# Kernel tuning notes

Hardware: AMD Instinct MI355X
Metric: run time of the kernel (lower is better)

Reference implementation:

```python
import jax, jax.numpy as jnp
import numpy as np
from jax import lax

B, D, H, W = 8, 256, 56, 56
DH = 32            # d_head
HEADS = D // DH    # 8
WIN = 7            # window size
TOPK = 8           # top-k windows
DM = 4 * D         # mlp hidden = 1024
EPS = 1e-5


def bn(x, g, b, m, v):
    # inference-mode BatchNorm2d over channel dim of NCHW
    return g[:, None, None] * (x - m[:, None, None]) * lax.rsqrt(v[:, None, None] + EPS) + b[:, None, None]


def conv1x1(x, w):
    return jnp.einsum('bchw,oc->bohw', x, w)


def setup_inputs() -> dict:
    key = jax.random.key(0)
    ks = jax.random.split(key, 24)
    s = 0.05
    return {
        'x': jax.random.normal(ks[0], (B, D, H, W), jnp.float32),
        'g1': jax.random.uniform(ks[1], (D,)) + 0.5,
        'b1': jax.random.normal(ks[2], (D,)) * s,
        'm1': jax.random.normal(ks[3], (D,)) * s,
        'v1': jax.random.uniform(ks[4], (D,)) + 0.5,
        'W_qkv': jax.random.normal(ks[5], (3 * D, D)) * s,
        'W_merge': jax.random.normal(ks[6], (D, D)) * s,
        'b_merge': jax.random.normal(ks[7], (D,)) * s,
        'W1': jax.random.normal(ks[8], (DM, D)) * s,
        'g2': jax.random.uniform(ks[9], (DM,)) + 0.5,
        'b2': jax.random.normal(ks[10], (DM,)) * s,
        'm2': jax.random.normal(ks[11], (DM,)) * s,
        'v2': jax.random.uniform(ks[12], (DM,)) + 0.5,
        'Wdw': jax.random.normal(ks[13], (DM, 1, 3, 3)) * s,
        'g3': jax.random.uniform(ks[14], (DM,)) + 0.5,
        'b3': jax.random.normal(ks[15], (DM,)) * s,
        'm3': jax.random.normal(ks[16], (DM,)) * s,
        'v3': jax.random.uniform(ks[17], (DM,)) + 0.5,
        'W2': jax.random.normal(ks[18], (D, DM)) * s,
        'g4': jax.random.uniform(ks[19], (D,)) + 0.5,
        'b4': jax.random.normal(ks[20], (D,)) * s,
        'm4': jax.random.normal(ks[21], (D,)) * s,
        'v4': jax.random.uniform(ks[22], (D,)) + 0.5,
    }


def _forward(x, g1, b1, m1, v1, W_qkv, W_merge, b_merge,
             W1, g2, b2, m2, v2, Wdw, g3, b3, m3, v3, W2, g4, b4, m4, v4):
    b_, d, Hh, Ww = x.shape
    nh, nw = Hh // WIN, Ww // WIN
    nWnd, ww = nh * nw, WIN * WIN

    # qkv projection: BN -> GELU -> 1x1 conv
    h = jax.nn.gelu(bn(x, g1, b1, m1, v1), approximate=False)
    qkv = conv1x1(h, W_qkv)
    q, k, v = jnp.split(qkv, 3, axis=1)  # each [b, d, H, W]

    def part(t):  # -> [b, heads, nWnd, ww, dh]
        t = t.reshape(b_, HEADS, DH, nh, WIN, nw, WIN)
        return jnp.transpose(t, (0, 1, 3, 5, 4, 6, 2)).reshape(b_, HEADS, nWnd, ww, DH)

    qw, kw, vw = part(q), part(k), part(v)

    # window-level routing: mean-pooled q/k per window, top-k window selection
    def pool(t):  # [b, d, H, W] -> [b, nWnd, d]
        t = t.reshape(b_, d, nh, WIN, nw, WIN).mean(axis=(3, 5))
        return t.reshape(b_, d, nWnd).transpose(0, 2, 1)

    qr, kr = pool(q), pool(k)
    aff = jnp.einsum('bnd,bmd->bnm', qr, kr)        # [b, nWnd, nWnd]
    idx = lax.top_k(aff, TOPK)[1]                    # [b, nWnd, TOPK]

    def gath(t, i):  # t [heads, nWnd, ww, dh], i [nWnd, TOPK]
        return t[:, i]  # [heads, nWnd, TOPK, ww, dh]

    kg = jax.vmap(gath)(kw, idx).reshape(b_, HEADS, nWnd, TOPK * ww, DH)
    vg = jax.vmap(gath)(vw, idx).reshape(b_, HEADS, nWnd, TOPK * ww, DH)

    scores = jnp.einsum('bhnqd,bhnkd->bhnqk', qw, kg) / jnp.sqrt(jnp.float32(DH))
    attn = jax.nn.softmax(scores, axis=-1)
    out = jnp.einsum('bhnqk,bhnkd->bhnqd', attn, vg)  # [b, heads, nWnd, ww, dh]

    # un-partition back to [b, d, H, W]
    out = out.reshape(b_, HEADS, nh, nw, WIN, WIN, DH)
    msg = jnp.transpose(out, (0, 1, 6, 2, 4, 3, 5)).reshape(b_, d, Hh, Ww)

    # merge (1x1 conv with bias) + residual
    x = x + conv1x1(msg, W_merge) + b_merge[None, :, None, None]

    # MB mlp block: 1x1 -> BN -> GELU -> dw3x3 -> BN -> GELU -> 1x1 -> BN
    h2 = conv1x1(x, W1)
    h2 = jax.nn.gelu(bn(h2, g2, b2, m2, v2), approximate=False)
    h2 = lax.conv_general_dilated(h2, Wdw, (1, 1), 'SAME',
                                  feature_group_count=DM,
                                  dimension_numbers=('NCHW', 'OIHW', 'NCHW'))
    h2 = jax.nn.gelu(bn(h2, g3, b3, m3, v3), approximate=False)
    h2 = conv1x1(h2, W2)
    h2 = bn(h2, g4, b4, m4, v4)
    return x + h2


def reference(x, g1, b1, m1, v1, W_qkv, W_merge, b_merge,
              W1, g2, b2, m2, v2, Wdw, g3, b3, m3, v3, W2, g4, b4, m4, v4):
    return _forward(x, g1, b1, m1, v1, W_qkv, W_merge, b_merge,
                    W1, g2, b2, m2, v2, Wdw, g3, b3, m3, v3, W2, g4, b4, m4, v4)
```

## Files before the change

kernel.cpp:

```cpp
#include <hip/hip_runtime.h>
#include <cstdint>
#include <cstddef>

#define BB 8
#define PP 3136
#define EPSV 1e-5f

using bf16x8 = __attribute__((ext_vector_type(8))) short;
using f32x4  = __attribute__((ext_vector_type(4))) float;

__device__ __forceinline__ float bf2f(unsigned short u) {
    union { float f; unsigned int i; } c; c.i = ((unsigned int)u) << 16; return c.f;
}
__device__ __forceinline__ unsigned short f2bf(float f) {
    union { float f; unsigned int i; } c; c.f = f;
    unsigned int r = c.i + 0x7FFFu + ((c.i >> 16) & 1u);
    return (unsigned short)(r >> 16);
}
__device__ __forceinline__ float gelu_f(float t) {
    return 0.5f * t * (1.0f + erff(t * 0.70710678118654752440f));
}
__device__ __forceinline__ void async16(const void* g, void* s) {
    __builtin_amdgcn_global_load_lds(
        (const __attribute__((address_space(1))) unsigned int*)g,
        (__attribute__((address_space(3))) unsigned int*)s, 16, 0, 0);
}

__global__ __launch_bounds__(256) void cvt_bf16_k(const float* __restrict__ src,
    unsigned short* __restrict__ dst, int n)
{
    int i = blockIdx.x * 256 + threadIdx.x;
    if (i < n) dst[i] = f2bf(src[i]);
}

__global__ __launch_bounds__(256) void transin_k(const float* __restrict__ x,
    const float* __restrict__ g1, const float* __restrict__ b1,
    const float* __restrict__ m1, const float* __restrict__ v1,
    float* __restrict__ x_pm, unsigned short* __restrict__ h_bf)
{
    __shared__ float tile[64][65];
    __shared__ float gam[64], bet[64], mu[64], rst[64];
    const int p0 = blockIdx.x * 64, c0 = blockIdx.y * 64, b = blockIdx.z;
    const int t = threadIdx.x;
    if (t < 64) { int c = c0 + t; gam[t] = g1[c]; bet[t] = b1[c]; mu[t] = m1[c]; rst[t] = rsqrtf(v1[c] + EPSV); }
    {
        int cl = t >> 2, px = (t & 3) * 16;
        const float* src = x + ((size_t)(b * 256 + c0 + cl)) * PP + p0 + px;
        #pragma unroll
        for (int i4 = 0; i4 < 4; i4++) {
            float4 r0 = *(const float4*)(src + i4 * 4);
            tile[cl][px + i4*4 + 0] = r0.x; tile[cl][px + i4*4 + 1] = r0.y;
            tile[cl][px + i4*4 + 2] = r0.z; tile[cl][px + i4*4 + 3] = r0.w;
        }
    }
    __syncthreads();
    {
        int pl = t >> 2, cb = (t & 3) * 16;
        float raw[16], hg[16];
        #pragma unroll
        for (int i = 0; i < 16; i++) {
            float vv = tile[cb + i][pl];
            raw[i] = vv;
            hg[i] = gelu_f(gam[cb + i] * (vv - mu[cb + i]) * rst[cb + i] + bet[cb + i]);
        }
        size_t off = ((size_t)b * PP + p0 + pl) * 256 + c0 + cb;
        float* xd = x_pm + off;
        #pragma unroll
        for (int i4 = 0; i4 < 4; i4++) {
            float4 o; o.x = raw[i4*4]; o.y = raw[i4*4+1]; o.z = raw[i4*4+2]; o.w = raw[i4*4+3];
            *(float4*)(xd + i4 * 4) = o;
        }
        unsigned int uw[8];
        #pragma unroll
        for (int j = 0; j < 8; j++)
            uw[j] = (unsigned int)f2bf(hg[2*j]) | ((unsigned int)f2bf(hg[2*j+1]) << 16);
        uint4* hd = (uint4*)(h_bf + off);
        uint4 h0; h0.x = uw[0]; h0.y = uw[1]; h0.z = uw[2]; h0.w = uw[3];
        uint4 h1; h1.x = uw[4]; h1.y = uw[5]; h1.z = uw[6]; h1.w = uw[7];
        hd[0] = h0; hd[1] = h1;
    }
}

template<int EPI>
__global__ __launch_bounds__(256) void gemm_mfma_k(
    const unsigned short* __restrict__ Aact,
    const unsigned short* __restrict__ Wbf,
    const int K, const int Mout,
    void* __restrict__ C1, void* __restrict__ C2,
    const float* __restrict__ e0, const float* __restrict__ e1,
    const float* __restrict__ e2, const float* __restrict__ e3,
    const float* __restrict__ resid)
{
    __shared__ __align__(16) unsigned short As[4][128 * 32];
    __shared__ __align__(16) unsigned short Bs[4][128 * 32];
    const int tid = threadIdx.x;
    const int w = tid >> 6, lane = tid & 63, g = lane >> 4, l15 = lane & 15;
    const int wm = w >> 1, wn = w & 1;
    const size_t row0 = (size_t)blockIdx.x * 128;
    const int n0 = blockIdx.y * 128;

    const int srow = tid >> 2;
    const int scb  = tid & 3;

    const f32x4 vzero = {0.f, 0.f, 0.f, 0.f};
    f32x4 acc[4][4];
    #pragma unroll
    for (int mf = 0; mf < 4; mf++)
        #pragma unroll
        for (int nf = 0; nf < 4; nf++) acc[mf][nf] = vzero;

    const int NT = K >> 5;

    auto STAGE = [&](int s) {
        const int k0 = s << 5;
        unsigned short* Ad = &As[s & 3][0];
        unsigned short* Bd = &Bs[s & 3][0];
        #pragma unroll
        for (int r = 0; r < 2; r++) {
            int row = r * 64 + srow;
            int cbp = scb ^ ((row >> 1) & 3);
            async16(Aact + (row0 + row) * K + k0 + cbp * 8, Ad + r * 2048 + w * 512);
            async16(Wbf + (size_t)(n0 + row) * K + k0 + cbp * 8, Bd + r * 2048 + w * 512);
        }
    };
    auto COMPUTE = [&](int t) {
        const unsigned short* Ab = As[t & 3];
        const unsigned short* Bb = Bs[t & 3];
        bf16x8 af[4], bfr[4];
        #pragma unroll
        for (int mf = 0; mf < 4; mf++) {
            int row = wm * 64 + mf * 16 + l15;
            int gb = g ^ ((row >> 1) & 3);
            af[mf] = *(const bf16x8*)&Ab[row * 32 + gb * 8];
        }
        #pragma unroll
        for (int nf = 0; nf < 4; nf++) {
            int row = wn * 64 + nf * 16 + l15;
            int gb = g ^ ((row >> 1) & 3);
            bfr[nf] = *(const bf16x8*)&Bb[row * 32 + gb * 8];
        }
        #pragma unroll
        for (int mf = 0; mf < 4; mf++)
            #pragma unroll
            for (int nf = 0; nf < 4; nf++)
                acc[mf][nf] = __builtin_amdgcn_mfma_f32_16x16x32_bf16(af[mf], bfr[nf], acc[mf][nf], 0, 0, 0);
    };

    STAGE(0); STAGE(1); STAGE(2);
    for (int t = 0; t < NT - 2; ++t) {
        asm volatile("s_waitcnt vmcnt(8)" ::: "memory");
        __builtin_amdgcn_s_barrier();
        if (t + 3 < NT) STAGE(t + 3);
        COMPUTE(t);
    }
    asm volatile("s_waitcnt vmcnt(4)" ::: "memory");
    __builtin_amdgcn_s_barrier();
    COMPUTE(NT - 2);
    asm volatile("s_waitcnt vmcnt(0)" ::: "memory");
    __builtin_amdgcn_s_barrier();
    COMPUTE(NT - 1);

    #pragma unroll
    for (int nf = 0; nf < 4; nf++) {
        const int mcol = n0 + wn * 64 + nf * 16 + l15;
        float gam = 0.f, bet = 0.f, mu = 0.f, rs = 0.f, bias = 0.f;
        if (EPI == 2 || EPI == 3) {
            gam = e0[mcol]; bet = e1[mcol]; mu = e2[mcol]; rs = rsqrtf(e3[mcol] + EPSV);
        }
        if (EPI == 1) bias = e0[mcol];
        #pragma unroll
        for (int mf = 0; mf < 4; mf++) {
            #pragma unroll
            for (int r = 0; r < 4; r++) {
                const size_t prow = row0 + wm * 64 + mf * 16 + g * 4 + r;
                const size_t off = prow * Mout + mcol;
                float a = acc[mf][nf][r];
                if (EPI == 0) {
                    if (mcol < 256) a *= 0.17677669529663687f;
                    ((unsigned short*)C1)[off] = f2bf(a);
                } else if (EPI == 1) {
                    float y = a + bias + resid[off];
                    ((float*)C1)[off] = y;
                    ((unsigned short*)C2)[off] = f2bf(y);
                } else if (EPI == 2) {
                    float y = gam * (a - mu) * rs + bet;
                    ((unsigned short*)C1)[off] = f2bf(gelu_f(y));
                } else {
                    float y = gam * (a - mu) * rs + bet + resid[off];
                    ((float*)C1)[off] = y;
                }
            }
        }
    }
}

__global__ __launch_bounds__(256) void poolh_k(const float* __restrict__ x_pm,
    const float* __restrict__ g1, const float* __restrict__ b1,
    const float* __restrict__ m1, const float* __restrict__ v1,
    float* __restrict__ ph)
{
    __shared__ float part[4][256];
    __shared__ float gam[256], bet[256], mu[256], rst[256];
    const int n = blockIdx.x, b = blockIdx.y, t = threadIdx.x;
    gam[t] = g1[t]; bet[t] = b1[t]; mu[t] = m1[t]; rst[t] = rsqrtf(v1[t] + EPSV);
    __syncthreads();
    const int c4 = (t & 63) * 4, pg = t >> 6;
    float s0 = 0.f, s1 = 0.f, s2 = 0.f, s3 = 0.f;
    for (int j = pg; j < 49; j += 4) {
        int p = ((n >> 3) * 7 + j / 7) * 56 + (n & 7) * 7 + j % 7;
        float4 vx = *(const float4*)(x_pm + ((size_t)b * PP + p) * 256 + c4);
        s0 += gelu_f(gam[c4+0] * (vx.x - mu[c4+0]) * rst[c4+0] + bet[c4+0]);
        s1 += gelu_f(gam[c4+1] * (vx.y - mu[c4+1]) * rst[c4+1] + bet[c4+1]);
        s2 += gelu_f(gam[c4+2] * (vx.z - mu[c4+2]) * rst[c4+2] + bet[c4+2]);
        s3 += gelu_f(gam[c4+3] * (vx.w - mu[c4+3]) * rst[c4+3] + bet[c4+3]);
    }
    part[pg][c4 + 0] = s0; part[pg][c4 + 1] = s1; part[pg][c4 + 2] = s2; part[pg][c4 + 3] = s3;
    __syncthreads();
    float tot = part[0][t] + part[1][t] + part[2][t] + part[3][t];
    ph[((size_t)b * 64 + n) * 256 + t] = tot * (1.0f / 49.0f);
}

__global__ __launch_bounds__(256) void qrkr_k(const float* __restrict__ ph,
    const float* __restrict__ Wqkv, float* __restrict__ qr, float* __restrict__ kr)
{
    __shared__ float row[256];
    const int n = blockIdx.x, b = blockIdx.y, t = threadIdx.x;
    row[t] = ph[((size_t)b * 64 + n) * 256 + t];
    __syncthreads();
    const float* wq = Wqkv + (size_t)t * 256;
    const float* wk = Wqkv + (size_t)(256 + t) * 256;
    float aq = 0.f, ak = 0.f;
    #pragma unroll 4
    for (int k = 0; k < 256; k += 4) {
        float4 a4 = *(const float4*)(wq + k);
        float4 b4 = *(const float4*)(wk + k);
        aq += row[k]*a4.x + row[k+1]*a4.y + row[k+2]*a4.z + row[k+3]*a4.w;
        ak += row[k]*b4.x + row[k+1]*b4.y + row[k+2]*b4.z + row[k+3]*b4.w;
    }
    qr[((size_t)b * 64 + n) * 256 + t] = aq;
    kr[((size_t)b * 64 + n) * 256 + t] = ak;
}

__global__ __launch_bounds__(64) void topk_k(const float* __restrict__ qr,
    const float* __restrict__ kr, int* __restrict__ idxb)
{
    const int n = blockIdx.x, b_ = blockIdx.y;
    const int tid = threadIdx.x;
    __shared__ float qrow[256];
    *reinterpret_cast<float4*>(&qrow[tid * 4]) =
        *reinterpret_cast<const float4*>(qr + ((size_t)(b_ * 64) + n) * 256 + tid * 4);
    __syncthreads();
    const float* kp = kr + ((size_t)(b_ * 64) + tid) * 256;
    float av = 0.f;
    #pragma unroll 4
    for (int c = 0; c < 256; c++) av = fmaf(qrow[c], kp[c], av);
    for (int t = 0; t < 8; t++) {
        float v = av; int id = tid;
        #pragma unroll
        for (int off = 32; off; off >>= 1) {
            float v2 = __shfl_xor(v, off);
            int id2 = __shfl_xor(id, off);
            if (v2 > v || (v2 == v && id2 < id)) { v = v2; id = id2; }
        }
        if (tid == 0) idxb[((b_ * 64) + n) * 8 + t] = id;
        if (tid == id) av = -1e30f;
    }
}

__global__ __launch_bounds__(256) void attn_mfma_k(const unsigned short* __restrict__ qkv,
    const int* __restrict__ idxb, unsigned short* __restrict__ msg)
{
    __shared__ __align__(16) unsigned short Ks[64 * 40];
    __shared__ __align__(16) unsigned short Vt[32 * 72];
    __shared__ __align__(16) unsigned short Pr[4][16 * 72];
    const int n = blockIdx.x, h = blockIdx.y, b = blockIdx.z;
    const int tid = threadIdx.x;
    const int w = tid >> 6, lane = tid & 63, g = lane >> 4, l15 = lane & 15;

    for (int e = tid; e < 64 * 40; e += 256) Ks[e] = 0;
    for (int e = tid; e < 32 * 72; e += 256) Vt[e] = 0;

    const int iq = w * 16 + l15;
    bf16x8 qf = {0, 0, 0, 0, 0, 0, 0, 0};
    if (iq < 49) {
        int p = ((n >> 3) * 7 + iq / 7) * 56 + (n & 7) * 7 + iq % 7;
        qf = *(const bf16x8*)(qkv + ((size_t)b * PP + p) * 768 + h * 32 + g * 8);
    }
    const f32x4 vzero = {0.f, 0.f, 0.f, 0.f};
    f32x4 o0 = vzero, o1 = vzero;
    float mrow = -1e30f, lrow = 0.f;

    for (int t = 0; t < 8; t++) {
        const int wsrc = idxb[((b * 64) + n) * 8 + t];
        const int sy0 = (wsrc >> 3) * 7, sx0 = (wsrc & 7) * 7;
        __syncthreads();
        if (tid < 196) {
            int j = tid >> 2, c8 = (tid & 3) * 8;
            int p = (sy0 + j / 7) * 56 + sx0 + j % 7;
            const unsigned short* srcp = qkv + ((size_t)b * PP + p) * 768 + 256 + h * 32 + c8;
            uint4 kk = *(const uint4*)srcp;
            *(uint4*)&Ks[j * 40 + c8] = kk;
            uint4 vv = *(const uint4*)(srcp + 256);
            const unsigned short* pv = (const unsigned short*)&vv;
            #pragma unroll
            for (int jj = 0; jj < 8; jj++) {
                int dh = c8 + jj;
                Vt[dh * 72 + (j ^ (((dh >> 3) & 3) << 3))] = pv[jj];
            }
        }
        __syncthreads();
        f32x4 s[4];
        #pragma unroll
        for (int nf = 0; nf < 4; nf++) {
            bf16x8 kf = *(const bf16x8*)&Ks[(nf * 16 + l15) * 40 + g * 8];
            s[nf] = __builtin_amdgcn_mfma_f32_16x16x32_bf16(kf, qf, vzero, 0, 0, 0);
        }
        float sv[16];
        #pragma unroll
        for (int nf = 0; nf < 4; nf++)
            #pragma unroll
            for (int r = 0; r < 4; r++) {
                int j = nf * 16 + g * 4 + r;
                sv[nf * 4 + r] = (j < 49) ? s[nf][r] : -1e30f;
            }
        float wmx = sv[0];
        #pragma unroll
        for (int e = 1; e < 16; e++) wmx = fmaxf(wmx, sv[e]);
        wmx = fmaxf(wmx, __shfl_xor(wmx, 16));
        wmx = fmaxf(wmx, __shfl_xor(wmx, 32));
        float mn = fmaxf(mrow, wmx);
        float corr = __expf(mrow - mn);
        mrow = mn;
        float rsum = 0.f;
        #pragma unroll
        for (int e = 0; e < 16; e++) { float pe = __expf(sv[e] - mn); sv[e] = pe; rsum += pe; }
        rsum += __shfl_xor(rsum, 16);
        rsum += __shfl_xor(rsum, 32);
        lrow = lrow * corr + rsum;
        #pragma unroll
        for (int r = 0; r < 4; r++) { o0[r] *= corr; o1[r] *= corr; }
        #pragma unroll
        for (int nf = 0; nf < 4; nf++) {
            uint2 pw;
            pw.x = (unsigned)f2bf(sv[nf*4+0]) | ((unsigned)f2bf(sv[nf*4+1]) << 16);
            pw.y = (unsigned)f2bf(sv[nf*4+2]) | ((unsigned)f2bf(sv[nf*4+3]) << 16);
            *(uint2*)&Pr[w][l15 * 72 + nf * 16 + g * 4] = pw;
        }
        asm volatile("s_waitcnt lgkmcnt(0)" ::: "memory");
        #pragma unroll
        for (int ks = 0; ks < 2; ks++) {
            const int j0 = ks * 32 + g * 8;
            bf16x8 pf  = *(const bf16x8*)&Pr[w][l15 * 72 + j0];
            bf16x8 vf0 = *(const bf16x8*)&Vt[l15 * 72 + (j0 ^ (((l15 >> 3) & 1) << 3))];
            bf16x8 vf1 = *(const bf16x8*)&Vt[(16 + l15) * 72 + (j0 ^ ((2 + (l15 >> 3)) << 3))];
            o0 = __builtin_amdgcn_mfma_f32_16x16x32_bf16(vf0, pf, o0, 0, 0, 0);
            o1 = __builtin_amdgcn_mfma_f32_16x16x32_bf16(vf1, pf, o1, 0, 0, 0);
        }
    }
    if (iq < 49) {
        float inv = 1.0f / lrow;
        int p = ((n >> 3) * 7 + iq / 7) * 56 + (n & 7) * 7 + iq % 7;
        size_t off = ((size_t)b * PP + p) * 256 + h * 32;
        uint2 w0, w1;
        w0.x = (unsigned)f2bf(o0[0]*inv) | ((unsigned)f2bf(o0[1]*inv) << 16);
        w0.y = (unsigned)f2bf(o0[2]*inv) | ((unsigned)f2bf(o0[3]*inv) << 16);
        w1.x = (unsigned)f2bf(o1[0]*inv) | ((unsigned)f2bf(o1[1]*inv) << 16);
        w1.y = (unsigned)f2bf(o1[2]*inv) | ((unsigned)f2bf(o1[3]*inv) << 16);
        *(uint2*)(msg + off + g * 4) = w0;
        *(uint2*)(msg + off + 16 + g * 4) = w1;
    }
}

__global__ __launch_bounds__(256) void dwconv_k(const unsigned short* __restrict__ in,
    const float* __restrict__ w9,
    const float* __restrict__ g3, const float* __restrict__ b3,
    const float* __restrict__ m3, const float* __restrict__ v3,
    unsigned short* __restrict__ out)
{
    __shared__ __align__(16) unsigned short tl[100 * 64];
    const int sx = blockIdx.x % 7, sy = blockIdx.x / 7;
    const int c0 = blockIdx.y * 64, b = blockIdx.z;
    const int t = threadIdx.x;
    for (int e = t; e < 800; e += 256) {
        int pos = e >> 3, c8 = (e & 7) * 8;
        int iy = sy * 8 + pos / 10 - 1, ix = sx * 8 + pos % 10 - 1;
        uint4 val = {0u, 0u, 0u, 0u};
        if (iy >= 0 && iy < 56 && ix >= 0 && ix < 56)
            val = *(const uint4*)(in + ((size_t)b * PP + iy * 56 + ix) * 1024 + c0 + c8);
        *(uint4*)&tl[pos * 64 + c8] = val;
    }
    __syncthreads();
    const int c2 = (t & 31) * 2, pg = t >> 5;
    const int c = c0 + c2;
    float w0[9], w1[9];
    #pragma unroll
    for (int i = 0; i < 9; i++) { w0[i] = w9[c * 9 + i]; w1[i] = w9[(c + 1) * 9 + i]; }
    const float ga0 = g3[c], be0 = b3[c], mu0 = m3[c], rs0 = rsqrtf(v3[c] + EPSV);
    const float ga1 = g3[c+1], be1 = b3[c+1], mu1 = m3[c+1], rs1 = rsqrtf(v3[c+1] + EPSV);
    #pragma unroll
    for (int q = 0; q < 8; q++) {
        int pos = pg * 8 + q, y = pos >> 3, xq = pos & 7;
        float s0 = 0.f, s1 = 0.f;
        #pragma unroll
        for (int dy = 0; dy < 3; dy++)
            #pragma unroll
            for (int dx = 0; dx < 3; dx++) {
                unsigned int u = *(const unsigned int*)&tl[((y + dy) * 10 + xq + dx) * 64 + c2];
                s0 = fmaf(bf2f((unsigned short)(u & 0xffffu)), w0[dy * 3 + dx], s0);
                s1 = fmaf(bf2f((unsigned short)(u >> 16)), w1[dy * 3 + dx], s1);
            }
        float y0 = gelu_f(ga0 * (s0 - mu0) * rs0 + be0);
        float y1 = gelu_f(ga1 * (s1 - mu1) * rs1 + be1);
        unsigned int ow = (unsigned int)f2bf(y0) | ((unsigned int)f2bf(y1) << 16);
        size_t off = ((size_t)b * PP + (sy * 8 + y) * 56 + sx * 8 + xq) * 1024 + c;
        *(unsigned int*)&out[off] = ow;
    }
}

__global__ __launch_bounds__(256) void transout_k(const float* __restrict__ out_pm,
    float* __restrict__ dout)
{
    __shared__ float tile[64][65];
    const int p0 = blockIdx.x * 64, c0 = blockIdx.y * 64, b = blockIdx.z;
    const int t = threadIdx.x;
    {
        int pl = t >> 2, cx = (t & 3) * 16;
        const float* src = out_pm + ((size_t)b * PP + p0 + pl) * 256 + c0 + cx;
        #pragma unroll
        for (int i4 = 0; i4 < 4; i4++) {
            float4 vv = *(const float4*)(src + i4 * 4);
            tile[pl][cx + i4*4 + 0] = vv.x; tile[pl][cx + i4*4 + 1] = vv.y;
            tile[pl][cx + i4*4 + 2] = vv.z; tile[pl][cx + i4*4 + 3] = vv.w;
        }
    }
    __syncthreads();
    {
        int cl = t >> 2, px = (t & 3) * 16;
        float* dst = dout + ((size_t)(b * 256 + c0 + cl)) * PP + p0 + px;
        #pragma unroll
        for (int i4 = 0; i4 < 4; i4++) {
            float4 o;
            o.x = tile[px + i4*4 + 0][cl]; o.y = tile[px + i4*4 + 1][cl];
            o.z = tile[px + i4*4 + 2][cl]; o.w = tile[px + i4*4 + 3][cl];
            *(float4*)(dst + i4 * 4) = o;
        }
    }
}

extern "C" void kernel_launch(void* const* d_in, const int* in_sizes, int n_in,
                              void* d_out, int out_size, void* d_ws, size_t ws_size,
                              hipStream_t stream)
{
    const float* x      = (const float*)d_in[0];
    const float* g1     = (const float*)d_in[1];
    const float* b1     = (const float*)d_in[2];
    const float* m1     = (const float*)d_in[3];
    const float* v1     = (const float*)d_in[4];
    const float* Wqkv   = (const float*)d_in[5];
    const float* Wmerge = (const float*)d_in[6];
    const float* bmerge = (const float*)d_in[7];
    const float* W1     = (const float*)d_in[8];
    const float* g2     = (const float*)d_in[9];
    const float* b2     = (const float*)d_in[10];
    const float* m2     = (const float*)d_in[11];
    const float* v2     = (const float*)d_in[12];
    const float* Wdw    = (const float*)d_in[13];
    const float* g3     = (const float*)d_in[14];
    const float* b3     = (const float*)d_in[15];
    const float* m3     = (const float*)d_in[16];
    const float* v3     = (const float*)d_in[17];
    const float* W2     = (const float*)d_in[18];
    const float* g4     = (const float*)d_in[19];
    const float* b4     = (const float*)d_in[20];
    const float* m4     = (const float*)d_in[21];
    const float* v4     = (const float*)d_in[22];

    char* ws = (char*)d_ws;
    float*          x_pm   = (float*)(ws + 0);
    float*          x2_pm  = (float*)(ws + 25690112);
    unsigned short* x2_bf  = (unsigned short*)(ws + 51380224);
    unsigned short* qkv_pm = (unsigned short*)(ws + 64225280);
    unsigned short* msg_pm = (unsigned short*)(ws + 102760448);
    unsigned short* t1     = (unsigned short*)(ws + 115605504);
    unsigned short* h_bf   = t1;
    unsigned short* t2     = (unsigned short*)(ws + 166985728);
    float*          ph     = (float*)(ws + 218365952);
    float*          qr     = (float*)(ws + 218890240);
    float*          kr     = (float*)(ws + 219414528);
    int*            idxb   = (int*)(ws + 219938816);
    unsigned short* Wqkv_b = (unsigned short*)(ws + 219955200);
    unsigned short* Wmrg_b = (unsigned short*)(ws + 220348416);
    unsigned short* W1_b   = (unsigned short*)(ws + 220479488);
    unsigned short* W2_b   = (unsigned short*)(ws + 221003776);
    float*          out_pm = x_pm;
    if (ws_size < 221528064) return;

    cvt_bf16_k<<<768, 256, 0, stream>>>(Wqkv, Wqkv_b, 196608);
    cvt_bf16_k<<<256, 256, 0, stream>>>(Wmerge, Wmrg_b, 65536);
    cvt_bf16_k<<<1024, 256, 0, stream>>>(W1, W1_b, 262144);
    cvt_bf16_k<<<1024, 256, 0, stream>>>(W2, W2_b, 262144);
    transin_k<<<dim3(49, 4, BB), 256, 0, stream>>>(x, g1, b1, m1, v1, x_pm, h_bf);
    gemm_mfma_k<0><<<dim3(196, 6), 256, 0, stream>>>(h_bf, Wqkv_b, 256, 768,
        qkv_pm, nullptr, nullptr, nullptr, nullptr, nullptr, nullptr);
    poolh_k<<<dim3(64, BB), 256, 0, stream>>>(x_pm, g1, b1, m1, v1, ph);
    qrkr_k<<<dim3(64, BB), 256, 0, stream>>>(ph, Wqkv, qr, kr);
    topk_k<<<dim3(64, BB), 64, 0, stream>>>(qr, kr, idxb);
    attn_mfma_k<<<dim3(64, 8, BB), 256, 0, stream>>>(qkv_pm, idxb, msg_pm);
    gemm_mfma_k<1><<<dim3(196, 2), 256, 0, stream>>>(msg_pm, Wmrg_b, 256, 256,
        x2_pm, x2_bf, bmerge, nullptr, nullptr, nullptr, x_pm);
    gemm_mfma_k<2><<<dim3(196, 8), 256, 0, stream>>>(x2_bf, W1_b, 256, 1024,
        t1, nullptr, g2, b2, m2, v2, nullptr);
    dwconv_k<<<dim3(49, 16, BB), 256, 0, stream>>>(t1, Wdw, g3, b3, m3, v3, t2);
    gemm_mfma_k<3><<<dim3(196, 2), 256, 0, stream>>>(t2, W2_b, 1024, 256,
        out_pm, nullptr, g4, b4, m4, v4, x2_pm);
    transout_k<<<dim3(49, 4, BB), 256, 0, stream>>>(out_pm, (float*)d_out);
}
```

Measured before the change: 345.5 us.

## Stage GEMM epilogue through LDS, use tanh GELU, fuse weight casts, prefetch attention K/V

Several changes at once. The GEMM epilogue now goes through shared memory so each thread writes contiguous 16-byte vectors instead of scattered 2/4-byte stores. The GEMM pipeline shrinks from 4-stage to 2-stage buffering with __syncthreads, which cuts LDS to about 34 KB but reduces the prefetch depth. Exact erf GELU is replaced by a tanh/sigmoid approximation in transin, the W1 epilogue and dwconv, which changes numerics. The four weight-conversion launches are merged into one, and the attention kernel prefetches the next window's K/V into registers while the current one is processed.

After: 340.9 us. About the same (-1.3%).

```diff
diff --git a/kernel.cpp b/kernel.cpp
--- a/kernel.cpp
+++ b/kernel.cpp
@@ -5,6 +5,7 @@
 #define BB 8
 #define PP 3136
 #define EPSV 1e-5f
+#define SCQK 0.17677669529663687f
 
 using bf16x8 = __attribute__((ext_vector_type(8))) short;
 using f32x4  = __attribute__((ext_vector_type(4))) float;
@@ -20,17 +21,35 @@
 __device__ __forceinline__ float gelu_f(float t) {
     return 0.5f * t * (1.0f + erff(t * 0.70710678118654752440f));
 }
+__device__ __forceinline__ float gelu_fast(float x) {
+    float z = 1.5957691216057308f * (x + 0.044715f * x * x * x);
+    return x / (1.0f + __expf(-z));
+}
 __device__ __forceinline__ void async16(const void* g, void* s) {
     __builtin_amdgcn_global_load_lds(
         (const __attribute__((address_space(1))) unsigned int*)g,
         (__attribute__((address_space(3))) unsigned int*)s, 16, 0, 0);
 }
-
-__global__ __launch_bounds__(256) void cvt_bf16_k(const float* __restrict__ src,
-    unsigned short* __restrict__ dst, int n)
+__device__ __forceinline__ uint4 pack8(const float* v) {
+    uint4 o;
+    o.x = (unsigned)f2bf(v[0]) | ((unsigned)f2bf(v[1]) << 16);
+    o.y = (unsigned)f2bf(v[2]) | ((unsigned)f2bf(v[3]) << 16);
+    o.z = (unsigned)f2bf(v[4]) | ((unsigned)f2bf(v[5]) << 16);
+    o.w = (unsigned)f2bf(v[6]) | ((unsigned)f2bf(v[7]) << 16);
+    return o;
+}
+
+__global__ __launch_bounds__(256) void cvt_all_k(
+    const float* __restrict__ Wq, const float* __restrict__ Wm,
+    const float* __restrict__ W1, const float* __restrict__ W2,
+    unsigned short* __restrict__ dq, unsigned short* __restrict__ dm,
+    unsigned short* __restrict__ d1, unsigned short* __restrict__ d2)
 {
     int i = blockIdx.x * 256 + threadIdx.x;
-    if (i < n) dst[i] = f2bf(src[i]);
+    if (i < 196608) dq[i] = f2bf(Wq[i]);
+    else if (i < 262144) dm[i - 196608] = f2bf(Wm[i - 196608]);
+    else if (i < 524288) d1[i - 262144] = f2bf(W1[i - 262144]);
+    else d2[i - 524288] = f2bf(W2[i - 524288]);
 }
 
 __global__ __launch_bounds__(256) void transin_k(const float* __restrict__ x,
@@ -61,7 +80,7 @@
         for (int i = 0; i < 16; i++) {
             float vv = tile[cb + i][pl];
             raw[i] = vv;
-            hg[i] = gelu_f(gam[cb + i] * (vv - mu[cb + i]) * rst[cb + i] + bet[cb + i]);
+            hg[i] = gelu_fast(gam[cb + i] * (vv - mu[cb + i]) * rst[cb + i] + bet[cb + i]);
         }
         size_t off = ((size_t)b * PP + p0 + pl) * 256 + c0 + cb;
         float* xd = x_pm + off;
@@ -70,14 +89,9 @@
             float4 o; o.x = raw[i4*4]; o.y = raw[i4*4+1]; o.z = raw[i4*4+2]; o.w = raw[i4*4+3];
             *(float4*)(xd + i4 * 4) = o;
         }
-        unsigned int uw[8];
-        #pragma unroll
-        for (int j = 0; j < 8; j++)
-            uw[j] = (unsigned int)f2bf(hg[2*j]) | ((unsigned int)f2bf(hg[2*j+1]) << 16);
         uint4* hd = (uint4*)(h_bf + off);
-        uint4 h0; h0.x = uw[0]; h0.y = uw[1]; h0.z = uw[2]; h0.w = uw[3];
-        uint4 h1; h1.x = uw[4]; h1.y = uw[5]; h1.z = uw[6]; h1.w = uw[7];
-        hd[0] = h0; hd[1] = h1;
+        hd[0] = pack8(&hg[0]);
+        hd[1] = pack8(&hg[8]);
     }
 }
 
@@ -91,16 +105,17 @@
     const float* __restrict__ e2, const float* __restrict__ e3,
     const float* __restrict__ resid)
 {
-    __shared__ __align__(16) unsigned short As[4][128 * 32];
-    __shared__ __align__(16) unsigned short Bs[4][128 * 32];
+    __shared__ __align__(16) char smem[34816];
+    unsigned short* As0 = (unsigned short*)smem;
+    unsigned short* Bs0 = (unsigned short*)(smem + 16384);
+    float* T = (float*)smem;
+
     const int tid = threadIdx.x;
     const int w = tid >> 6, lane = tid & 63, g = lane >> 4, l15 = lane & 15;
     const int wm = w >> 1, wn = w & 1;
     const size_t row0 = (size_t)blockIdx.x * 128;
     const int n0 = blockIdx.y * 128;
-
-    const int srow = tid >> 2;
-    const int scb  = tid & 3;
+    const int srow = tid >> 2, scb = tid & 3;
 
     const f32x4 vzero = {0.f, 0.f, 0.f, 0.f};
     f32x4 acc[4][4];
@@ -113,8 +128,8 @@
 
     auto STAGE = [&](int s) {
         const int k0 = s << 5;
-        unsigned short* Ad = &As[s & 3][0];
-        unsigned short* Bd = &Bs[s & 3][0];
+        unsigned short* Ad = As0 + (s & 1) * 4096;
+        unsigned short* Bd = Bs0 + (s & 1) * 4096;
         #pragma unroll
         for (int r = 0; r < 2; r++) {
             int row = r * 64 + srow;
@@ -124,8 +139,8 @@
         }
     };
     auto COMPUTE = [&](int t) {
-        const unsigned short* Ab = As[t & 3];
-        const unsigned short* Bb = Bs[t & 3];
+        const unsigned short* Ab = As0 + (t & 1) * 4096;
+        const unsigned short* Bb = Bs0 + (t & 1) * 4096;
         bf16x8 af[4], bfr[4];
         #pragma unroll
         for (int mf = 0; mf < 4; mf++) {
@@ -146,49 +161,95 @@
                 acc[mf][nf] = __builtin_amdgcn_mfma_f32_16x16x32_bf16(af[mf], bfr[nf], acc[mf][nf], 0, 0, 0);
     };
 
-    STAGE(0); STAGE(1); STAGE(2);
-    for (int t = 0; t < NT - 2; ++t) {
-        asm volatile("s_waitcnt vmcnt(8)" ::: "memory");
-        __builtin_amdgcn_s_barrier();
-        if (t + 3 < NT) STAGE(t + 3);
+    STAGE(0);
+    for (int t = 0; t < NT; ++t) {
+        __syncthreads();
+        if (t + 1 < NT) STAGE(t + 1);
         COMPUTE(t);
     }
-    asm volatile("s_waitcnt vmcnt(4)" ::: "memory");
-    __builtin_amdgcn_s_barrier();
-    COMPUTE(NT - 2);
-    asm volatile("s_waitcnt vmcnt(0)" ::: "memory");
-    __builtin_amdgcn_s_barrier();
-    COMPUTE(NT - 1);
-
+
+    __syncthreads();
+    const int erow = tid >> 1;
+    const int ec0 = (tid & 1) * 32;
     #pragma unroll
-    for (int nf = 0; nf < 4; nf++) {
-        const int mcol = n0 + wn * 64 + nf * 16 + l15;
-        float gam = 0.f, bet = 0.f, mu = 0.f, rs = 0.f, bias = 0.f;
-        if (EPI == 2 || EPI == 3) {
-            gam = e0[mcol]; bet = e1[mcol]; mu = e2[mcol]; rs = rsqrtf(e3[mcol] + EPSV);
-        }
-        if (EPI == 1) bias = e0[mcol];
-        #pragma unroll
-        for (int mf = 0; mf < 4; mf++) {
-            #pragma unroll
-            for (int r = 0; r < 4; r++) {
-                const size_t prow = row0 + wm * 64 + mf * 16 + g * 4 + r;
-                const size_t off = prow * Mout + mcol;
-                float a = acc[mf][nf][r];
-                if (EPI == 0) {
-                    if (mcol < 256) a *= 0.17677669529663687f;
-                    ((unsigned short*)C1)[off] = f2bf(a);
-                } else if (EPI == 1) {
-                    float y = a + bias + resid[off];
-                    ((float*)C1)[off] = y;
-                    ((unsigned short*)C2)[off] = f2bf(y);
-                } else if (EPI == 2) {
-                    float y = gam * (a - mu) * rs + bet;
-                    ((unsigned short*)C1)[off] = f2bf(gelu_f(y));
-                } else {
-                    float y = gam * (a - mu) * rs + bet + resid[off];
-                    ((float*)C1)[off] = y;
-                }
+    for (int pass = 0; pass < 2; ++pass) {
+        if (pass) __syncthreads();
+        if (wn == pass) {
+            #pragma unroll
+            for (int mf = 0; mf < 4; mf++)
+                #pragma unroll
+                for (int nf = 0; nf < 4; nf++)
+                    #pragma unroll
+                    for (int r = 0; r < 4; r++)
+                        T[(wm * 64 + mf * 16 + g * 4 + r) * 68 + nf * 16 + l15] = acc[mf][nf][r];
+        }
+        __syncthreads();
+        float vals[32];
+        #pragma unroll
+        for (int i = 0; i < 8; i++) {
+            float4 v = *(const float4*)&T[erow * 68 + ec0 + i * 4];
+            vals[i*4+0] = v.x; vals[i*4+1] = v.y; vals[i*4+2] = v.z; vals[i*4+3] = v.w;
+        }
+        const size_t prow = row0 + erow;
+        const int mc0 = n0 + pass * 64 + ec0;
+        const size_t off = prow * Mout + mc0;
+        if (EPI == 0) {
+            const float s = (mc0 < 256) ? SCQK : 1.0f;
+            #pragma unroll
+            for (int j = 0; j < 32; j++) vals[j] *= s;
+            uint4* dst = (uint4*)((unsigned short*)C1 + off);
+            #pragma unroll
+            for (int i = 0; i < 4; i++) dst[i] = pack8(&vals[i * 8]);
+        } else if (EPI == 1) {
+            #pragma unroll
+            for (int i = 0; i < 8; i++) {
+                float4 bi = *(const float4*)(e0 + mc0 + i * 4);
+                float4 rr = *(const float4*)(resid + off + i * 4);
+                vals[i*4+0] += bi.x + rr.x; vals[i*4+1] += bi.y + rr.y;
+                vals[i*4+2] += bi.z + rr.z; vals[i*4+3] += bi.w + rr.w;
+            }
+            float4* d1 = (float4*)((float*)C1 + off);
+            #pragma unroll
+            for (int i = 0; i < 8; i++) {
+                float4 o; o.x = vals[i*4]; o.y = vals[i*4+1]; o.z = vals[i*4+2]; o.w = vals[i*4+3];
+                d1[i] = o;
+            }
+            uint4* d2 = (uint4*)((unsigned short*)C2 + off);
+            #pragma unroll
+            for (int i = 0; i < 4; i++) d2[i] = pack8(&vals[i * 8]);
+        } else if (EPI == 2) {
+            #pragma unroll
+            for (int i = 0; i < 8; i++) {
+                float4 ga = *(const float4*)(e0 + mc0 + i * 4);
+                float4 be = *(const float4*)(e1 + mc0 + i * 4);
+                float4 mm = *(const float4*)(e2 + mc0 + i * 4);
+                float4 vv = *(const float4*)(e3 + mc0 + i * 4);
+                vals[i*4+0] = gelu_fast(ga.x * (vals[i*4+0] - mm.x) * rsqrtf(vv.x + EPSV) + be.x);
+                vals[i*4+1] = gelu_fast(ga.y * (vals[i*4+1] - mm.y) * rsqrtf(vv.y + EPSV) + be.y);
+                vals[i*4+2] = gelu_fast(ga.z * (vals[i*4+2] - mm.z) * rsqrtf(vv.z + EPSV) + be.z);
+                vals[i*4+3] = gelu_fast(ga.w * (vals[i*4+3] - mm.w) * rsqrtf(vv.w + EPSV) + be.w);
+            }
+            uint4* dst = (uint4*)((unsigned short*)C1 + off);
+            #pragma unroll
+            for (int i = 0; i < 4; i++) dst[i] = pack8(&vals[i * 8]);
+        } else {
+            #pragma unroll
+            for (int i = 0; i < 8; i++) {
+                float4 ga = *(const float4*)(e0 + mc0 + i * 4);
+                float4 be = *(const float4*)(e1 + mc0 + i * 4);
+                float4 mm = *(const float4*)(e2 + mc0 + i * 4);
+                float4 vv = *(const float4*)(e3 + mc0 + i * 4);
+                float4 rr = *(const float4*)(resid + off + i * 4);
+                vals[i*4+0] = ga.x * (vals[i*4+0] - mm.x) * rsqrtf(vv.x + EPSV) + be.x + rr.x;
+                vals[i*4+1] = ga.y * (vals[i*4+1] - mm.y) * rsqrtf(vv.y + EPSV) + be.y + rr.y;
+                vals[i*4+2] = ga.z * (vals[i*4+2] - mm.z) * rsqrtf(vv.z + EPSV) + be.z + rr.z;
+                vals[i*4+3] = ga.w * (vals[i*4+3] - mm.w) * rsqrtf(vv.w + EPSV) + be.w + rr.w;
+            }
+            float4* d1 = (float4*)((float*)C1 + off);
+            #pragma unroll
+            for (int i = 0; i < 8; i++) {
+                float4 o; o.x = vals[i*4]; o.y = vals[i*4+1]; o.z = vals[i*4+2]; o.w = vals[i*4+3];
+                d1[i] = o;
             }
         }
     }
@@ -290,23 +351,29 @@
     f32x4 o0 = vzero, o1 = vzero;
     float mrow = -1e30f, lrow = 0.f;
 
+    const bool act = tid < 196;
+    const int jrow = tid >> 2, c8 = (tid & 3) * 8;
+    uint4 kk_r = {0,0,0,0}, vv_r = {0,0,0,0};
+    auto LOADW = [&](int t) {
+        int wsrc = idxb[((b * 64) + n) * 8 + t];
+        int p = ((wsrc >> 3) * 7 + jrow / 7) * 56 + (wsrc & 7) * 7 + jrow % 7;
+        const unsigned short* srcp = qkv + ((size_t)b * PP + p) * 768 + 256 + h * 32 + c8;
+        kk_r = *(const uint4*)srcp;
+        vv_r = *(const uint4*)(srcp + 256);
+    };
+    if (act) LOADW(0);
+
     for (int t = 0; t < 8; t++) {
-        const int wsrc = idxb[((b * 64) + n) * 8 + t];
-        const int sy0 = (wsrc >> 3) * 7, sx0 = (wsrc & 7) * 7;
         __syncthreads();
-        if (tid < 196) {
-            int j = tid >> 2, c8 = (tid & 3) * 8;
-            int p = (sy0 + j / 7) * 56 + sx0 + j % 7;
-            const unsigned short* srcp = qkv + ((size_t)b * PP + p) * 768 + 256 + h * 32 + c8;
-            uint4 kk = *(const uint4*)srcp;
-            *(uint4*)&Ks[j * 40 + c8] = kk;
-            uint4 vv = *(const uint4*)(srcp + 256);
-            const unsigned short* pv = (const unsigned short*)&vv;
+        if (act) {
+            *(uint4*)&Ks[jrow * 40 + c8] = kk_r;
+            const unsigned short* pv = (const unsigned short*)&vv_r;
             #pragma unroll
             for (int jj = 0; jj < 8; jj++) {
                 int dh = c8 + jj;
-                Vt[dh * 72 + (j ^ (((dh >> 3) & 3) << 3))] = pv[jj];
-            }
+                Vt[dh * 72 + (jrow ^ (((dh >> 3) & 3) << 3))] = pv[jj];
+            }
+            if (t < 7) LOADW(t + 1);
         }
         __syncthreads();
         f32x4 s[4];
@@ -409,8 +476,8 @@
                 s0 = fmaf(bf2f((unsigned short)(u & 0xffffu)), w0[dy * 3 + dx], s0);
                 s1 = fmaf(bf2f((unsigned short)(u >> 16)), w1[dy * 3 + dx], s1);
             }
-        float y0 = gelu_f(ga0 * (s0 - mu0) * rs0 + be0);
-        float y1 = gelu_f(ga1 * (s1 - mu1) * rs1 + be1);
+        float y0 = gelu_fast(ga0 * (s0 - mu0) * rs0 + be0);
+        float y1 = gelu_fast(ga1 * (s1 - mu1) * rs1 + be1);
         unsigned int ow = (unsigned int)f2bf(y0) | ((unsigned int)f2bf(y1) << 16);
         size_t off = ((size_t)b * PP + (sy * 8 + y) * 56 + sx * 8 + xq) * 1024 + c;
         *(unsigned int*)&out[off] = ow;
@@ -495,10 +562,7 @@
     float*          out_pm = x_pm;
     if (ws_size < 221528064) return;
 
-    cvt_bf16_k<<<768, 256, 0, stream>>>(Wqkv, Wqkv_b, 196608);
-    cvt_bf16_k<<<256, 256, 0, stream>>>(Wmerge, Wmrg_b, 65536);
-    cvt_bf16_k<<<1024, 256, 0, stream>>>(W1, W1_b, 262144);
-    cvt_bf16_k<<<1024, 256, 0, stream>>>(W2, W2_b, 262144);
+    cvt_all_k<<<3072, 256, 0, stream>>>(Wqkv, Wmerge, W1, W2, Wqkv_b, Wmrg_b, W1_b, W2_b);
     transin_k<<<dim3(49, 4, BB), 256, 0, stream>>>(x, g1, b1, m1, v1, x_pm, h_bf);
     gemm_mfma_k<0><<<dim3(196, 6), 256, 0, stream>>>(h_bf, Wqkv_b, 256, 768,
         qkv_pm, nullptr, nullptr, nullptr, nullptr, nullptr, nullptr);
```
